# Performance work log

Hardware: AMD Instinct MI355X
Metric: run time of the kernel (lower is better)

The kernel has to match this reference:

```python
import jax, jax.numpy as jnp
import numpy as np

D = 4          # guide-feature dimension (in_channels_feature)
NV = D + 1     # simplex vertices / lattice remainders
BASE = 128     # per-coordinate key encoding base
OFF = 64
SENT = np.int32(2 ** 30)  # sentinel hash for unused slots


def _elevation_matrix(d):
    # Adams et al. elevation: cf = f * scale; elevated = E @ cf, built densely.
    E = np.zeros((d + 1, d), np.float32)
    E[0, :] = 1.0
    for i in range(1, d + 1):
        E[i, i - 1] = -i
        E[i, i:] = 1.0
    scale = 1.0 / np.sqrt((np.arange(d) + 1.0) * (np.arange(d) + 2.0))
    scale = scale * (d + 1.0) * np.sqrt(2.0 / 3.0)  # inv_std_dev
    return (E * scale[None, :]).astype(np.float32)


def _neighbor_offsets(d):
    # lattice axis vectors u_j (first d coords): u_j[i] = d if i==j else -1
    U = -np.ones((d + 1, d), np.int64)
    for j in range(d):
        U[j, j] = d
    offs = []
    for m in range(2 ** (d + 1) - 1):  # all subsets of axes except the full set
        c = [(m >> j) & 1 for j in range(d + 1)]
        offs.append(sum(c[j] * U[j] for j in range(d + 1)))
    return np.stack(offs).astype(np.int32)  # (F, d), F = 2^(d+1)-1


_EMB = jnp.asarray(_elevation_matrix(D))          # (NV, D)
_OFFS = jnp.asarray(_neighbor_offsets(D))         # (F, D)
_POW = jnp.asarray((BASE ** np.arange(D)).astype(np.int32))


def _encode(keys):  # (..., D) int32 -> (...,) int32 perfect hash within range
    k = jnp.clip(keys, -OFF, OFF - 1) + OFF
    return (k * _POW).sum(-1)


def _lattice_filter(feat, dat, Wk):
    # feat: (N, D) guide features; dat: (N, Cin); Wk: (Cout, Cin, F)
    N = feat.shape[0]
    M0 = N * NV  # max distinct lattice points
    elev = feat @ _EMB.T                      # (N, NV)
    g = jnp.round(elev / NV) * NV             # nearest remainder-0 point
    gi = jnp.round(g).astype(jnp.int32)
    s = gi.sum(-1) // NV                      # exact: coords are multiples of NV
    diff = elev - g
    order = jnp.argsort(-diff, axis=-1)       # stable descending sort of residuals
    rank = jnp.argsort(order, axis=-1).astype(jnp.int32) + s[:, None]
    low, high = rank < 0, rank > D
    rank = jnp.where(low, rank + NV, jnp.where(high, rank - NV, rank))
    gi = jnp.where(low, gi + NV, jnp.where(high, gi - NV, gi))
    t = (elev - gi.astype(elev.dtype)) / NV
    rows = jnp.arange(N)[:, None]
    bary = jnp.zeros((N, D + 2), elev.dtype)
    bary = bary.at[rows, D - rank].add(t)
    bary = bary.at[rows, NV - rank].add(1.0 - t)
    bary = bary.at[:, 0].add(1.0 + bary[:, D + 1])
    bary = bary[:, :NV]                       # (N, NV) barycentric weights
    # simplex vertex keys, first D coords only (last is -sum)
    kk = jnp.arange(NV, dtype=jnp.int32)[None, :, None]       # vertex color
    add = jnp.where(rank[:, None, :D] >= NV - kk, kk - NV, kk)
    keys = gi[:, None, :D] + add              # (N, NV, D)
    codes = _encode(keys)                     # (N, NV)
    # --- dedup lattice points (sort + first-occurrence ranks) ---
    flat = codes.reshape(-1)
    sortv = jnp.sort(flat)
    is_new = jnp.concatenate([jnp.ones((1,), bool), sortv[1:] != sortv[:-1]])
    urank = jnp.cumsum(is_new) - 1
    uniq = jnp.full((M0,), SENT, jnp.int32).at[urank].set(sortv)  # sorted uniques
    idx = jnp.searchsorted(uniq, flat)        # (M0,) slot of each (point,vertex)
    # --- splat ---
    Cin = dat.shape[1]
    vals = (dat[:, None, :] * bary[:, :, None]).reshape(M0, Cin)
    table = jnp.zeros((M0, Cin), dat.dtype).at[idx].add(vals)
    ukeys = jnp.zeros((M0, D), jnp.int32).at[idx].set(keys.reshape(M0, D))
    # --- blur: learned conv over lattice neighborhood ---
    ncodes = _encode(ukeys[:, None, :] + _OFFS[None, :, :])   # (M0, F)
    pos = jnp.clip(jnp.searchsorted(uniq, ncodes), 0, M0 - 1)
    valid = (uniq[pos] == ncodes)[..., None]
    gathered = table[pos] * valid             # (M0, F, Cin)
    out_lat = jnp.einsum('mfc,ocf->mo', gathered, Wk)  # (M0, Cout)
    # --- slice ---
    out = jnp.einsum('nk,nko->no', bary, out_lat[idx.reshape(N, NV)])
    return out  # (N, Cout)


def setup_inputs() -> dict:
    key = jax.random.key(0)
    k1, k2, k3, k4 = jax.random.split(key, 4)
    B, Cin, Cout, H, W = 4, 64, 64, 32, 32
    F = 2 ** (D + 1) - 1  # 31 = get_filter_size(1, D)
    return {
        'data': jax.random.normal(k1, (B, Cin, H, W), jnp.float32),
        'features': jax.random.normal(k2, (B, D, H, W), jnp.float32),
        'weights': 0.02 * jax.random.normal(k3, (Cout, Cin, 1, F), jnp.float32),
        'bias': 0.1 * jax.random.normal(k4, (1, 1, 1, Cout), jnp.float32),
        'bias_multiplier': jnp.ones((1, 1, 1, H * W), jnp.float32),
    }


def reference(data, features, weights, bias, bias_multiplier):
    B, Cin, H, W = data.shape
    N = H * W
    feat = features.reshape(B, D, N).transpose(0, 2, 1)   # (B, N, D)
    dat = data.reshape(B, Cin, N).transpose(0, 2, 1)      # (B, N, Cin)
    Wk = weights[:, :, 0, :]                              # (Cout, Cin, F)
    out = jax.vmap(lambda f, x: _lattice_filter(f, x, Wk))(feat, dat)  # (B, N, Cout)
    out = out + bias.reshape(-1)[None, None, :] * bias_multiplier.reshape(-1)[None, :, None]
    Cout = Wk.shape[0]
    return out.transpose(0, 2, 1).reshape(B, Cout, H, W)
```

## Files before the change

### kernel.cpp

```cpp
#include <hip/hip_runtime.h>
#include <hip/hip_bf16.h>
#include <stdint.h>

#define DD 4
#define NVERT 5
#define NPTS 1024
#define BATCH 4
#define M0 5120
#define CIN 64
#define COUT 64
#define NF 31
#define KTOT 1984
#define CAP 16384
#define CAPMASK (CAP-1)
#define SENTV 1073741824
#define ZROW (BATCH*M0)

using bf16x8 = __attribute__((ext_vector_type(8))) short;
using f32x4  = __attribute__((ext_vector_type(4))) float;

__device__ __forceinline__ unsigned short f2bf(float x){
  unsigned int u = __float_as_uint(x);
  u = (u + 0x7FFFu + ((u >> 16) & 1u)) >> 16;
  return (unsigned short)u;
}

__device__ __forceinline__ uint32_t hslot(int code){
  return (((uint32_t)code * 2654435761u) >> 18) & CAPMASK;
}

__device__ __forceinline__ void pv_math(const float* feat, int g, int* code_out, float* bary_out){
  int p = g / NVERT, kk = g % NVERT;
  int b = p >> 10, n = p & 1023;
  const float* fb = feat + (size_t)b * DD * NPTS + n;
  float f0 = fb[0], f1 = fb[NPTS], f2 = fb[2 * NPTS], f3 = fb[3 * NPTS];

  float elev[5];
  elev[0] =  f0 * 2.886751345948129f  + f1 * 1.6666666666666667f + f2 * 1.1785113019775793f + f3 * 0.9128709291752769f;
  elev[1] = -f0 * 2.886751345948129f  + f1 * 1.6666666666666667f + f2 * 1.1785113019775793f + f3 * 0.9128709291752769f;
  elev[2] =  f1 * -3.3333333333333335f + f2 * 1.1785113019775793f + f3 * 0.9128709291752769f;
  elev[3] =  f2 * -3.535533905932738f  + f3 * 0.9128709291752769f;
  elev[4] =  f3 * -3.6514837167011076f;

  int gi[5]; float diff[5]; int sum = 0;
  #pragma unroll
  for (int i = 0; i < 5; i++){
    float gg = rintf(elev[i] * 0.2f) * 5.0f;
    gi[i] = (int)rintf(gg);
    sum += gi[i];
    diff[i] = elev[i] - gg;
  }
  int s = sum / 5;

  int rank[5];
  #pragma unroll
  for (int i = 0; i < 5; i++){
    int r = 0;
    #pragma unroll
    for (int j = 0; j < 5; j++)
      r += (diff[j] > diff[i]) || (diff[j] == diff[i] && j < i);
    rank[i] = r + s;
  }
  #pragma unroll
  for (int i = 0; i < 5; i++){
    if (rank[i] < 0)      { rank[i] += NVERT; gi[i] += NVERT; }
    else if (rank[i] > DD){ rank[i] -= NVERT; gi[i] -= NVERT; }
  }

  float bary[6] = {0.f,0.f,0.f,0.f,0.f,0.f};
  #pragma unroll
  for (int i = 0; i < 5; i++){
    float tt = (elev[i] - (float)gi[i]) * 0.2f;
    bary[DD - rank[i]]    += tt;
    bary[NVERT - rank[i]] += 1.0f - tt;
  }
  bary[0] += 1.0f + bary[5];

  float bk = bary[0];
  #pragma unroll
  for (int i = 1; i < 5; i++) if (i == kk) bk = bary[i];

  int code = 0;
  #pragma unroll
  for (int j = 0; j < DD; j++){
    int add = (rank[j] >= NVERT - kk) ? (kk - NVERT) : kk;
    int key = gi[j] + add;
    key = min(63, max(-64, key));
    code += (key + 64) << (7 * j);
  }
  *code_out = code;
  *bary_out = bk;
}

__global__ void k_a(const float* __restrict__ wk, const float* __restrict__ data,
                    const float* __restrict__ feat,
                    int* __restrict__ hc, int* __restrict__ hu, int* __restrict__ uc,
                    float4* __restrict__ table4, float4* __restrict__ outlat4,
                    unsigned short* __restrict__ bpf, float* __restrict__ dat_t,
                    int* __restrict__ codes_pv, float* __restrict__ bary_pv){
  int bid = blockIdx.x, tid = threadIdx.x;
  if (bid < 64){
    __shared__ float tile[64][65];
    int b = bid >> 4, n0 = (bid & 15) * 64;
    int nl = tid & 63;
    #pragma unroll
    for (int i = 0; i < 16; i++){
      int c = (tid >> 6) * 16 + i;
      tile[c][nl] = data[(((size_t)b * 64 + c) << 10) + n0 + nl];
    }
    __syncthreads();
    #pragma unroll
    for (int i = 0; i < 16; i++){
      int nn = (tid >> 6) * 16 + i;
      dat_t[(((size_t)b << 10) + n0 + nn) * 64 + (tid & 63)] = tile[tid & 63][nn];
    }
  } else if (bid < 144){
    int g = (bid - 64) * 256 + tid;
    int code; float bk;
    pv_math(feat, g, &code, &bk);
    codes_pv[g] = code;
    bary_pv[g]  = bk;
  } else if (bid < 640){
    int e = (bid - 144) * 256 + tid;
    int frag = e >> 9, l = (e >> 3) & 63, j = e & 7;
    int f = frag >> 3, h = (frag >> 2) & 1, g = frag & 3;
    int col = g * 16 + (l & 15);
    int c = h * 32 + ((l >> 4) << 3) + j;
    bpf[e] = f2bf(wk[(col * CIN + c) * NF + f]);
  } else {
    int g = (bid - 640) * 256 + tid;
    int stride = 384 * 256;
    for (int i = g; i < BATCH * CAP; i += stride){ hc[i] = SENTV; hu[i] = -1; }
    if (g < BATCH) uc[g] = 0;
    float4 z = {0.f,0.f,0.f,0.f};
    for (int i = g; i < BATCH * M0 * CIN / 4; i += stride) table4[i] = z;
    for (int i = g; i < BATCH * M0 * COUT / 4; i += stride) outlat4[i] = z;
  }
}

__global__ void k_insert(const int* __restrict__ codes_pv,
                         int* __restrict__ hash_code, int* __restrict__ hash_uid,
                         int* __restrict__ ucount, int* __restrict__ ukeys){
  __shared__ int lhash[512];
  int tid = threadIdx.x;
  lhash[tid] = SENTV; lhash[tid + 256] = SENTV;
  __syncthreads();

  int g = blockIdx.x * 256 + tid;
  int b = g / M0;
  int code = codes_pv[g];

  uint32_t lh = (((uint32_t)code * 2654435761u) >> 21) & 511;
  bool rep = false;
  while (true){
    int prev = atomicCAS(&lhash[lh], SENTV, code);
    if (prev == SENTV){ rep = true; break; }
    if (prev == code) break;
    lh = (lh + 1) & 511;
  }

  int myslot = -1;
  if (rep){
    int* hc = hash_code + b * CAP;
    uint32_t h = hslot(code);
    while (true){
      int prev = atomicCAS(&hc[h], SENTV, code);
      if (prev == SENTV){ myslot = (int)h; break; }
      if (prev == code) break;
      h = (h + 1) & CAPMASK;
    }
  }

  unsigned long long mask = __ballot(myslot >= 0);
  if (mask){
    int lane = tid & 63;
    int cnt = __popcll(mask);
    int leader = __ffsll((unsigned long long)mask) - 1;
    int base = 0;
    if (lane == leader) base = atomicAdd(&ucount[b], cnt);
    base = __shfl(base, leader);
    if (myslot >= 0){
      int rank = __popcll(mask & ((1ull << lane) - 1ull));
      int uid = base + rank;
      hash_uid[b * CAP + myslot] = uid;
      int* uk = ukeys + ((size_t)(b * M0 + uid)) * DD;
      #pragma unroll
      for (int j = 0; j < DD; j++) uk[j] = ((code >> (7 * j)) & 127) - 64;
    }
  }
}

__global__ void k_sn(const float* __restrict__ dat_t, const int* __restrict__ codes_pv,
                     const float* __restrict__ bary_pv, const int* __restrict__ hash_code,
                     const int* __restrict__ hash_uid, const int* __restrict__ ucount,
                     const int* __restrict__ ukeys,
                     int* __restrict__ idx_pv, float* __restrict__ table,
                     int* __restrict__ nuid){
  int bid = blockIdx.x, tid = threadIdx.x;
  if (bid < BATCH * NPTS / 4){
    __shared__ int   us[4][8];
    __shared__ float wbs[4][8];
    int w = tid >> 6, lane = tid & 63;
    int p = bid * 4 + w;
    int b = p >> 10;
    float v = dat_t[((size_t)p << 6) + lane];
    if (lane < NVERT){
      int code = codes_pv[p * NVERT + lane];
      const int* hc = hash_code + b * CAP;
      uint32_t h = hslot(code);
      while (hc[h] != code) h = (h + 1) & CAPMASK;
      int uid = hash_uid[b * CAP + h];
      us[w][lane]  = uid;
      wbs[w][lane] = bary_pv[p * NVERT + lane];
      idx_pv[p * NVERT + lane] = uid;
    }
    __syncthreads();
    int rot = p % NVERT;
    #pragma unroll
    for (int kq = 0; kq < NVERT; kq++){
      int kk = kq + rot; if (kk >= NVERT) kk -= NVERT;
      atomicAdd(&table[(((size_t)(b * M0 + us[w][kk])) << 6) + lane], v * wbs[w][kk]);
    }
  } else {
    int e = (bid - BATCH * NPTS / 4) * 256 + tid;
    int f = e & 31;
    int idx = e >> 5;
    int b = idx / M0, m = idx - b * M0;
    int g = ZROW;
    if (f < NF && m < ucount[b]){
      const int* uk = ukeys + ((size_t)idx) * DD;
      int pc = __popc(f);
      int code = 0;
      #pragma unroll
      for (int j = 0; j < DD; j++){
        int key = uk[j] + 5 * ((f >> j) & 1) - pc;
        key = min(63, max(-64, key));
        code += (key + 64) << (7 * j);
      }
      const int* hc = hash_code + b * CAP;
      uint32_t h = hslot(code);
      while (true){
        int v = hc[h];
        if (v == code){ g = b * M0 + hash_uid[b * CAP + h]; break; }
        if (v == SENTV) break;
        h = (h + 1) & CAPMASK;
      }
    }
    nuid[e] = g;
  }
}

__global__ void k_tobf(const float* __restrict__ table, const int* __restrict__ ucount,
                       unsigned short* __restrict__ table_bf){
  int g = blockIdx.x * blockDim.x + threadIdx.x;
  if (g < 8){
    bf16x8 z = {0,0,0,0,0,0,0,0};
    *(bf16x8*)(table_bf + ((size_t)ZROW << 6) + g * 8) = z;
  }
  int row = g >> 3;
  int b = row / M0;
  if (row - b * M0 >= ucount[b]) return;
  size_t base = (size_t)g * 8;
  const float4* s4 = (const float4*)(table + base);
  float4 x = s4[0], y = s4[1];
  bf16x8 v;
  v[0] = (short)f2bf(x.x); v[1] = (short)f2bf(x.y);
  v[2] = (short)f2bf(x.z); v[3] = (short)f2bf(x.w);
  v[4] = (short)f2bf(y.x); v[5] = (short)f2bf(y.y);
  v[6] = (short)f2bf(y.z); v[7] = (short)f2bf(y.w);
  *(bf16x8*)(table_bf + base) = v;
}

__launch_bounds__(512, 4)
__global__ void k_conv(const int* __restrict__ ucount, const int* __restrict__ nuid,
                       const unsigned short* __restrict__ table_bf,
                       const unsigned short* __restrict__ bpf,
                       float* __restrict__ out_lat){
  __shared__ int gidx_s[64 * 33];
  __shared__ float red[7][64][17];

  int blk = blockIdx.x;
  int b    = blk / 160;
  int r    = blk % 160;
  int m0   = (r >> 1) * 64;
  int half = r & 1;
  if (m0 >= ucount[b]) return;

  int tid = threadIdx.x;
  {
    int base = (b * M0 + m0) << 5;
    #pragma unroll
    for (int i = 0; i < 4; i++){
      int idx = tid + i * 512;
      gidx_s[(idx >> 5) * 33 + (idx & 31)] = nuid[base + idx];
    }
  }
  __syncthreads();

  int lane = tid & 63, wave = tid >> 6;
  int rl = lane & 15;
  int acol = (lane >> 4) * 8;
  const unsigned short* bf_lane = bpf + ((size_t)lane << 3);

  f32x4 acc[4][4];
  #pragma unroll
  for (int rg = 0; rg < 4; rg++)
    #pragma unroll
    for (int g = 0; g < 4; g++)
      acc[rg][g] = (f32x4){0.f,0.f,0.f,0.f};

  int f0 = half * 16 + wave * 2;
  int f1 = f0 + 2; if (f1 > NF) f1 = NF;

  for (int f = f0; f < f1; f++){
    bf16x8 A0_0, A0_1, A1_0, A1_1, A2_0, A2_1, A3_0, A3_1;
    {
      const unsigned short* p0 = table_bf + (((size_t)gidx_s[(rl     ) * 33 + f]) << 6) + acol;
      const unsigned short* p1 = table_bf + (((size_t)gidx_s[(rl + 16) * 33 + f]) << 6) + acol;
      const unsigned short* p2 = table_bf + (((size_t)gidx_s[(rl + 32) * 33 + f]) << 6) + acol;
      const unsigned short* p3 = table_bf + (((size_t)gidx_s[(rl + 48) * 33 + f]) << 6) + acol;
      A0_0 = *(const bf16x8*)(p0); A0_1 = *(const bf16x8*)(p0 + 32);
      A1_0 = *(const bf16x8*)(p1); A1_1 = *(const bf16x8*)(p1 + 32);
      A2_0 = *(const bf16x8*)(p2); A2_1 = *(const bf16x8*)(p2 + 32);
      A3_0 = *(const bf16x8*)(p3); A3_1 = *(const bf16x8*)(p3 + 32);
    }
    int fr = f << 3;
    #pragma unroll
    for (int g = 0; g < 4; g++){
      bf16x8 B0 = *(const bf16x8*)(bf_lane + ((size_t)(fr + g)     << 9));
      bf16x8 B1 = *(const bf16x8*)(bf_lane + ((size_t)(fr + 4 + g) << 9));
      acc[0][g] = __builtin_amdgcn_mfma_f32_16x16x32_bf16(A0_0, B0, acc[0][g], 0, 0, 0);
      acc[0][g] = __builtin_amdgcn_mfma_f32_16x16x32_bf16(A0_1, B1, acc[0][g], 0, 0, 0);
      acc[1][g] = __builtin_amdgcn_mfma_f32_16x16x32_bf16(A1_0, B0, acc[1][g], 0, 0, 0);
      acc[1][g] = __builtin_amdgcn_mfma_f32_16x16x32_bf16(A1_1, B1, acc[1][g], 0, 0, 0);
      acc[2][g] = __builtin_amdgcn_mfma_f32_16x16x32_bf16(A2_0, B0, acc[2][g], 0, 0, 0);
      acc[2][g] = __builtin_amdgcn_mfma_f32_16x16x32_bf16(A2_1, B1, acc[2][g], 0, 0, 0);
      acc[3][g] = __builtin_amdgcn_mfma_f32_16x16x32_bf16(A3_0, B0, acc[3][g], 0, 0, 0);
      acc[3][g] = __builtin_amdgcn_mfma_f32_16x16x32_bf16(A3_1, B1, acc[3][g], 0, 0, 0);
    }
  }

  #pragma unroll
  for (int rg = 0; rg < 4; rg++){
    if (wave > 0){
      #pragma unroll
      for (int g = 0; g < 4; g++)
        #pragma unroll
        for (int q = 0; q < 4; q++)
          red[wave - 1][lane][g * 4 + q] = acc[rg][g][q];
    }
    __syncthreads();
    if (wave == 0){
      #pragma unroll
      for (int w = 0; w < 7; w++)
        #pragma unroll
        for (int g = 0; g < 4; g++)
          #pragma unroll
          for (int q = 0; q < 4; q++)
            acc[rg][g][q] += red[w][lane][g * 4 + q];
    }
    __syncthreads();
  }

  if (wave == 0){
    int q4 = (lane >> 4) * 4, col = lane & 15;
    #pragma unroll
    for (int rg = 0; rg < 4; rg++){
      #pragma unroll
      for (int q = 0; q < 4; q++){
        int m = m0 + rg * 16 + q4 + q;
        float* orow = out_lat + (((size_t)(b * M0 + m)) << 6);
        #pragma unroll
        for (int g = 0; g < 4; g++){
          atomicAdd(&orow[g * 16 + col], acc[rg][g][q]);
        }
      }
    }
  }
}

__global__ void k_slice(const float* __restrict__ bary_pv, const int* __restrict__ idx_pv,
                        const float* __restrict__ out_lat, const float* __restrict__ bias,
                        const float* __restrict__ bmul, float* __restrict__ out){
  __shared__ float tile[16][65];
  int b = blockIdx.x >> 6, n0 = (blockIdx.x & 63) * 16;
  int tid = threadIdx.x;
  int wave = tid >> 6, o = tid & 63;
  float bo = bias[o];
  #pragma unroll
  for (int i = 0; i < 4; i++){
    int n = wave * 4 + i;
    int p = (b << 10) + n0 + n;
    float acc = bo * bmul[n0 + n];
    int base = p * NVERT;
    #pragma unroll
    for (int kk = 0; kk < NVERT; kk++){
      int u = idx_pv[base + kk];
      acc += bary_pv[base + kk] * out_lat[(((size_t)(b * M0 + u)) << 6) + o];
    }
    tile[n][o] = acc;
  }
  __syncthreads();
  int nl = tid & 15;
  #pragma unroll
  for (int i = 0; i < 4; i++){
    int o2 = (tid >> 4) + i * 16;
    out[(((size_t)b * 64 + o2) << 10) + n0 + nl] = tile[nl][o2];
  }
}

extern "C" void kernel_launch(void* const* d_in, const int* in_sizes, int n_in,
                              void* d_out, int out_size, void* d_ws, size_t ws_size,
                              hipStream_t stream){
  const float* data = (const float*)d_in[0];
  const float* feat = (const float*)d_in[1];
  const float* wk   = (const float*)d_in[2];
  const float* bias = (const float*)d_in[3];
  const float* bmul = (const float*)d_in[4];
  float* out = (float*)d_out;

  char* ws = (char*)d_ws;
  size_t off = 0;
  auto alloc = [&](size_t bytes){
    void* p = ws + off;
    off = (off + bytes + 255) & ~(size_t)255;
    return p;
  };
  int*   codes_pv = (int*)  alloc((size_t)BATCH * M0 * 4);
  float* bary_pv  = (float*)alloc((size_t)BATCH * M0 * 4);
  int*   idx_pv   = (int*)  alloc((size_t)BATCH * M0 * 4);
  int*   hash_code= (int*)  alloc((size_t)BATCH * CAP * 4);
  int*   hash_uid = (int*)  alloc((size_t)BATCH * CAP * 4);
  int*   ucount   = (int*)  alloc(256);
  int*   ukeys    = (int*)  alloc((size_t)BATCH * M0 * DD * 4);
  float* table    = (float*)alloc((size_t)BATCH * M0 * CIN * 4);
  float* out_lat  = (float*)alloc((size_t)BATCH * M0 * COUT * 4);
  unsigned short* bpf      = (unsigned short*)alloc((size_t)COUT * KTOT * 2);
  unsigned short* table_bf = (unsigned short*)alloc(((size_t)BATCH * M0 + 8) * CIN * 2);
  float* dat_t    = (float*)alloc((size_t)BATCH * NPTS * CIN * 4);
  int*   nuid     = (int*)  alloc((size_t)BATCH * M0 * 32 * 4);

  k_a     <<<1024, 256, 0, stream>>>(wk, data, feat, hash_code, hash_uid, ucount,
                                     (float4*)table, (float4*)out_lat, bpf, dat_t,
                                     codes_pv, bary_pv);
  k_insert<<<BATCH * M0 / 256, 256, 0, stream>>>(codes_pv, hash_code, hash_uid, ucount, ukeys);
  k_sn    <<<BATCH * NPTS / 4 + BATCH * M0 * 32 / 256, 256, 0, stream>>>(
            dat_t, codes_pv, bary_pv, hash_code, hash_uid, ucount, ukeys,
            idx_pv, table, nuid);
  k_tobf  <<<BATCH * M0 * CIN / 8 / 256, 256, 0, stream>>>(table, ucount, table_bf);
  k_conv  <<<BATCH * 160, 512, 0, stream>>>(ucount, nuid, table_bf, bpf, out_lat);
  k_slice <<<BATCH * 64, 256, 0, stream>>>(bary_pv, idx_pv, out_lat, bias, bmul, out);
}
```

Baseline: 41.86 us.

## Fuse neighbor hash lookup into conv kernel, drop nuid buffer

Moves the per-lattice-point neighbor lookup (key offset, hash probe) from the k_sn kernel into the k_conv prologue. Each conv block now computes only the 16 filter taps it needs for its 64 rows and keeps them in shared memory, so the global nuid array is no longer written and read back. This shrinks k_sn's grid and removes that round trip through memory, but adds hash-probe latency to the start of each conv block, before its MFMA work can begin.

```diff
diff --git a/kernel.cpp b/kernel.cpp
--- a/kernel.cpp
+++ b/kernel.cpp
@@ -192,61 +192,31 @@
 
 __global__ void k_sn(const float* __restrict__ dat_t, const int* __restrict__ codes_pv,
                      const float* __restrict__ bary_pv, const int* __restrict__ hash_code,
-                     const int* __restrict__ hash_uid, const int* __restrict__ ucount,
-                     const int* __restrict__ ukeys,
-                     int* __restrict__ idx_pv, float* __restrict__ table,
-                     int* __restrict__ nuid){
-  int bid = blockIdx.x, tid = threadIdx.x;
-  if (bid < BATCH * NPTS / 4){
-    __shared__ int   us[4][8];
-    __shared__ float wbs[4][8];
-    int w = tid >> 6, lane = tid & 63;
-    int p = bid * 4 + w;
-    int b = p >> 10;
-    float v = dat_t[((size_t)p << 6) + lane];
-    if (lane < NVERT){
-      int code = codes_pv[p * NVERT + lane];
-      const int* hc = hash_code + b * CAP;
-      uint32_t h = hslot(code);
-      while (hc[h] != code) h = (h + 1) & CAPMASK;
-      int uid = hash_uid[b * CAP + h];
-      us[w][lane]  = uid;
-      wbs[w][lane] = bary_pv[p * NVERT + lane];
-      idx_pv[p * NVERT + lane] = uid;
-    }
-    __syncthreads();
-    int rot = p % NVERT;
-    #pragma unroll
-    for (int kq = 0; kq < NVERT; kq++){
-      int kk = kq + rot; if (kk >= NVERT) kk -= NVERT;
-      atomicAdd(&table[(((size_t)(b * M0 + us[w][kk])) << 6) + lane], v * wbs[w][kk]);
-    }
-  } else {
-    int e = (bid - BATCH * NPTS / 4) * 256 + tid;
-    int f = e & 31;
-    int idx = e >> 5;
-    int b = idx / M0, m = idx - b * M0;
-    int g = ZROW;
-    if (f < NF && m < ucount[b]){
-      const int* uk = ukeys + ((size_t)idx) * DD;
-      int pc = __popc(f);
-      int code = 0;
-      #pragma unroll
-      for (int j = 0; j < DD; j++){
-        int key = uk[j] + 5 * ((f >> j) & 1) - pc;
-        key = min(63, max(-64, key));
-        code += (key + 64) << (7 * j);
-      }
-      const int* hc = hash_code + b * CAP;
-      uint32_t h = hslot(code);
-      while (true){
-        int v = hc[h];
-        if (v == code){ g = b * M0 + hash_uid[b * CAP + h]; break; }
-        if (v == SENTV) break;
-        h = (h + 1) & CAPMASK;
-      }
-    }
-    nuid[e] = g;
+                     const int* __restrict__ hash_uid,
+                     int* __restrict__ idx_pv, float* __restrict__ table){
+  __shared__ int   us[4][8];
+  __shared__ float wbs[4][8];
+  int tid = threadIdx.x;
+  int w = tid >> 6, lane = tid & 63;
+  int p = blockIdx.x * 4 + w;
+  int b = p >> 10;
+  float v = dat_t[((size_t)p << 6) + lane];
+  if (lane < NVERT){
+    int code = codes_pv[p * NVERT + lane];
+    const int* hc = hash_code + b * CAP;
+    uint32_t h = hslot(code);
+    while (hc[h] != code) h = (h + 1) & CAPMASK;
+    int uid = hash_uid[b * CAP + h];
+    us[w][lane]  = uid;
+    wbs[w][lane] = bary_pv[p * NVERT + lane];
+    idx_pv[p * NVERT + lane] = uid;
+  }
+  __syncthreads();
+  int rot = p % NVERT;
+  #pragma unroll
+  for (int kq = 0; kq < NVERT; kq++){
+    int kk = kq + rot; if (kk >= NVERT) kk -= NVERT;
+    atomicAdd(&table[(((size_t)(b * M0 + us[w][kk])) << 6) + lane], v * wbs[w][kk]);
   }
 }
 
@@ -272,11 +242,13 @@
 }
 
 __launch_bounds__(512, 4)
-__global__ void k_conv(const int* __restrict__ ucount, const int* __restrict__ nuid,
+__global__ void k_conv(const int* __restrict__ ucount, const int* __restrict__ ukeys,
+                       const int* __restrict__ hash_code, const int* __restrict__ hash_uid,
                        const unsigned short* __restrict__ table_bf,
                        const unsigned short* __restrict__ bpf,
                        float* __restrict__ out_lat){
-  __shared__ int gidx_s[64 * 33];
+  __shared__ int uk_s[64][4];
+  __shared__ int gidx_s[64 * 17];
   __shared__ float red[7][64][17];
 
   int blk = blockIdx.x;
@@ -284,15 +256,44 @@
   int r    = blk % 160;
   int m0   = (r >> 1) * 64;
   int half = r & 1;
-  if (m0 >= ucount[b]) return;
+  int ucnt = ucount[b];
+  if (m0 >= ucnt) return;
 
   int tid = threadIdx.x;
+  if (tid < 256){
+    int row = tid >> 2, j = tid & 3;
+    uk_s[row][j] = ukeys[((size_t)(b * M0 + m0 + row)) * DD + j];
+  }
+  __syncthreads();
+
   {
-    int base = (b * M0 + m0) << 5;
-    #pragma unroll
-    for (int i = 0; i < 4; i++){
-      int idx = tid + i * 512;
-      gidx_s[(idx >> 5) * 33 + (idx & 31)] = nuid[base + idx];
+    const int* hc = hash_code + b * CAP;
+    const int* hu = hash_uid  + b * CAP;
+    #pragma unroll
+    for (int it = 0; it < 2; it++){
+      int li = tid + it * 512;
+      int row = li & 63, fl = li >> 6;
+      int f = half * 16 + fl;
+      int m = m0 + row;
+      int g = ZROW;
+      if (f < NF && m < ucnt){
+        int pc = __popc(f);
+        int code = 0;
+        #pragma unroll
+        for (int j = 0; j < DD; j++){
+          int key = uk_s[row][j] + 5 * ((f >> j) & 1) - pc;
+          key = min(63, max(-64, key));
+          code += (key + 64) << (7 * j);
+        }
+        uint32_t h = hslot(code);
+        while (true){
+          int v = hc[h];
+          if (v == code){ g = b * M0 + hu[h]; break; }
+          if (v == SENTV) break;
+          h = (h + 1) & CAPMASK;
+        }
+      }
+      gidx_s[row * 17 + fl] = g;
     }
   }
   __syncthreads();
@@ -313,12 +314,13 @@
   int f1 = f0 + 2; if (f1 > NF) f1 = NF;
 
   for (int f = f0; f < f1; f++){
+    int fl = f - half * 16;
     bf16x8 A0_0, A0_1, A1_0, A1_1, A2_0, A2_1, A3_0, A3_1;
     {
-      const unsigned short* p0 = table_bf + (((size_t)gidx_s[(rl     ) * 33 + f]) << 6) + acol;
-      const unsigned short* p1 = table_bf + (((size_t)gidx_s[(rl + 16) * 33 + f]) << 6) + acol;
-      const unsigned short* p2 = table_bf + (((size_t)gidx_s[(rl + 32) * 33 + f]) << 6) + acol;
-      const unsigned short* p3 = table_bf + (((size_t)gidx_s[(rl + 48) * 33 + f]) << 6) + acol;
+      const unsigned short* p0 = table_bf + (((size_t)gidx_s[(rl     ) * 17 + fl]) << 6) + acol;
+      const unsigned short* p1 = table_bf + (((size_t)gidx_s[(rl + 16) * 17 + fl]) << 6) + acol;
+      const unsigned short* p2 = table_bf + (((size_t)gidx_s[(rl + 32) * 17 + fl]) << 6) + acol;
+      const unsigned short* p3 = table_bf + (((size_t)gidx_s[(rl + 48) * 17 + fl]) << 6) + acol;
       A0_0 = *(const bf16x8*)(p0); A0_1 = *(const bf16x8*)(p0 + 32);
       A1_0 = *(const bf16x8*)(p1); A1_1 = *(const bf16x8*)(p1 + 32);
       A2_0 = *(const bf16x8*)(p2); A2_1 = *(const bf16x8*)(p2 + 32);
@@ -438,16 +440,15 @@
   unsigned short* bpf      = (unsigned short*)alloc((size_t)COUT * KTOT * 2);
   unsigned short* table_bf = (unsigned short*)alloc(((size_t)BATCH * M0 + 8) * CIN * 2);
   float* dat_t    = (float*)alloc((size_t)BATCH * NPTS * CIN * 4);
-  int*   nuid     = (int*)  alloc((size_t)BATCH * M0 * 32 * 4);
 
   k_a     <<<1024, 256, 0, stream>>>(wk, data, feat, hash_code, hash_uid, ucount,
                                      (float4*)table, (float4*)out_lat, bpf, dat_t,
                                      codes_pv, bary_pv);
   k_insert<<<BATCH * M0 / 256, 256, 0, stream>>>(codes_pv, hash_code, hash_uid, ucount, ukeys);
-  k_sn    <<<BATCH * NPTS / 4 + BATCH * M0 * 32 / 256, 256, 0, stream>>>(
-            dat_t, codes_pv, bary_pv, hash_code, hash_uid, ucount, ukeys,
-            idx_pv, table, nuid);
+  k_sn    <<<BATCH * NPTS / 4, 256, 0, stream>>>(dat_t, codes_pv, bary_pv,
+                                                 hash_code, hash_uid, idx_pv, table);
   k_tobf  <<<BATCH * M0 * CIN / 8 / 256, 256, 0, stream>>>(table, ucount, table_bf);
-  k_conv  <<<BATCH * 160, 512, 0, stream>>>(ucount, nuid, table_bf, bpf, out_lat);
+  k_conv  <<<BATCH * 160, 512, 0, stream>>>(ucount, ukeys, hash_code, hash_uid,
+                                            table_bf, bpf, out_lat);
   k_slice <<<BATCH * 64, 256, 0, stream>>>(bary_pv, idx_pv, out_lat, bias, bmul, out);
 }
```

Result: no change. 42.52 us (+1.6%).
